# Optimization experiments

Measured on AMD Instinct MI355X. Metric: run time of the kernel, lower is better.

Reference implementation:

```python
import jax, jax.numpy as jnp
import numpy as np

B, S, D = 2, 2048, 1024
H = 16
HD = D // H
MLP = 4096
EPS_LN = 1e-6
EPS_NORM = 1e-12
LOG_MAX = float(np.log(1.0 / 0.01))  # clamp cap for logit_scale


def setup_inputs() -> dict:
    key = jax.random.key(0)
    ks = jax.random.split(key, 12)
    sd = 0.02
    return {
        "x": jax.random.normal(ks[0], (B, S, D), jnp.float32),
        "wq": jax.random.normal(ks[1], (D, D), jnp.float32) * sd,
        "bq": jnp.zeros((D,), jnp.float32),
        "wk": jax.random.normal(ks[2], (D, D), jnp.float32) * sd,
        "bk": jnp.zeros((D,), jnp.float32),
        "wv": jax.random.normal(ks[3], (D, D), jnp.float32) * sd,
        "bv": jnp.zeros((D,), jnp.float32),
        "wo": jax.random.normal(ks[4], (D, D), jnp.float32) * sd,
        "bo": jnp.zeros((D,), jnp.float32),
        "w1": jax.random.normal(ks[5], (D, MLP), jnp.float32) * sd,
        "b1": jax.random.normal(ks[6], (MLP,), jnp.float32) * 1e-6,
        "w2": jax.random.normal(ks[7], (MLP, D), jnp.float32) * sd,
        "b2": jax.random.normal(ks[8], (D,), jnp.float32) * 1e-6,
        "ln1_g": jnp.ones((D,), jnp.float32),
        "ln1_b": jnp.zeros((D,), jnp.float32),
        "ln2_g": jnp.ones((D,), jnp.float32),
        "ln2_b": jnp.zeros((D,), jnp.float32),
        "logit_scale": jnp.log(10.0 * jnp.ones((H, 1, 1), jnp.float32)),
    }


def _layernorm(x, g, b):
    mu = jnp.mean(x, axis=-1, keepdims=True)
    var = jnp.var(x, axis=-1, keepdims=True)
    return (x - mu) * jax.lax.rsqrt(var + EPS_LN) * g + b


def _l2norm(x):
    n = jnp.linalg.norm(x, axis=-1, keepdims=True)
    return x / jnp.maximum(n, EPS_NORM)


def _split_heads(t):  # [B,S,D] -> [B,H,S,HD]
    return t.reshape(B, S, H, HD).transpose(0, 2, 1, 3)


def reference(x, wq, bq, wk, bk, wv, bv, wo, bo, w1, b1, w2, b2,
              ln1_g, ln1_b, ln2_g, ln2_b, logit_scale):
    h = x
    xn = _layernorm(x, ln1_g, ln1_b)
    q = _split_heads(xn @ wq + bq)
    k = _split_heads(xn @ wk + bk)
    v = _split_heads(xn @ wv + bv)
    # cosine attention: L2-normalize q,k, scale by clamped learnable exp temp
    scores = jnp.einsum("bhqd,bhkd->bhqk", _l2norm(q), _l2norm(k))
    scale = jnp.exp(jnp.minimum(logit_scale, LOG_MAX))  # [H,1,1]
    scores = scores * scale
    probs = jax.nn.softmax(scores, axis=-1)
    ctx = jnp.einsum("bhqk,bhkd->bhqd", probs, v)
    ctx = ctx.transpose(0, 2, 1, 3).reshape(B, S, D)
    x = ctx @ wo + bo + h
    h = x
    xn = _layernorm(x, ln2_g, ln2_b)
    y = jax.nn.gelu(xn @ w1 + b1, approximate=False) @ w2 + b2
    return y + h
```

## Files before the change

### kernel.cpp

```cpp
#include <hip/hip_runtime.h>
#include <hip/hip_bf16.h>
#include <math.h>

typedef unsigned short u16;
typedef unsigned int u32;
typedef __attribute__((ext_vector_type(8))) short bf16x8;
typedef __attribute__((ext_vector_type(4))) float f32x4;

#define S_LEN 2048
#define DM 1024
#define NH 16
#define HD 64
#define MLPD 4096
#define BSZ 2
#define NROWS (BSZ * S_LEN)
#define LOGMAX 4.60517018598809f

__device__ __forceinline__ u16 f2bf(float f) {
  u32 u = __float_as_uint(f);
  u32 r = (u + 0x7fffu + ((u >> 16) & 1u)) >> 16;
  return (u16)r;
}
__device__ __forceinline__ float bf2f(u16 h) { return __uint_as_float(((u32)h) << 16); }
__device__ __forceinline__ u32 pk2(float a, float b) {
  return (u32)f2bf(a) | ((u32)f2bf(b) << 16);
}
__device__ __forceinline__ void gld16(const void* g, void* l) {
  __builtin_amdgcn_global_load_lds(
      (const __attribute__((address_space(1))) void*)g,
      (__attribute__((address_space(3))) void*)l, 16, 0, 0);
}

__global__ __launch_bounds__(256) void ln_bf16(const float* __restrict__ x,
                                               const float* __restrict__ g,
                                               const float* __restrict__ b,
                                               u16* __restrict__ out) {
  const int row = blockIdx.x;
  const int t = threadIdx.x;
  const float* xr = x + (size_t)row * DM;
  float4 v = *reinterpret_cast<const float4*>(xr + t * 4);
  float s = v.x + v.y + v.z + v.w;
  float s2 = v.x * v.x + v.y * v.y + v.z * v.z + v.w * v.w;
#pragma unroll
  for (int off = 32; off > 0; off >>= 1) {
    s += __shfl_down(s, off);
    s2 += __shfl_down(s2, off);
  }
  __shared__ float red[8];
  __shared__ float mv[2];
  const int wid = t >> 6, lane = t & 63;
  if (lane == 0) { red[wid] = s; red[wid + 4] = s2; }
  __syncthreads();
  if (t == 0) {
    float ts = red[0] + red[1] + red[2] + red[3];
    float ts2 = red[4] + red[5] + red[6] + red[7];
    float mu = ts * (1.0f / DM);
    float var = ts2 * (1.0f / DM) - mu * mu;
    mv[0] = mu;
    mv[1] = rsqrtf(var + 1e-6f);
  }
  __syncthreads();
  const float mu = mv[0], rs = mv[1];
  float4 gv = *reinterpret_cast<const float4*>(g + t * 4);
  float4 bv = *reinterpret_cast<const float4*>(b + t * 4);
  float o0 = (v.x - mu) * rs * gv.x + bv.x;
  float o1 = (v.y - mu) * rs * gv.y + bv.y;
  float o2 = (v.z - mu) * rs * gv.z + bv.z;
  float o3 = (v.w - mu) * rs * gv.w + bv.w;
  uint2 o;
  o.x = pk2(o0, o1);
  o.y = pk2(o2, o3);
  *reinterpret_cast<uint2*>(out + (size_t)row * DM + t * 4) = o;
}

__global__ __launch_bounds__(256) void prep_weights(
    const float* __restrict__ wq, const float* __restrict__ wk, const float* __restrict__ wv,
    const float* __restrict__ wo, const float* __restrict__ w1, const float* __restrict__ w2,
    const float* __restrict__ bq, const float* __restrict__ bk, const float* __restrict__ bv,
    u16* __restrict__ wqkv_t, u16* __restrict__ wo_t, u16* __restrict__ w1_t,
    u16* __restrict__ w2_t, float* __restrict__ bqkv) {
  const int tid = threadIdx.x;
  int bid = blockIdx.x;
  if (bid < 12) {
    int i = bid * 256 + tid;
    bqkv[i] = i < 1024 ? bq[i] : (i < 2048 ? bk[i - 1024] : bv[i - 2048]);
  }
  const float* src;
  u16* dst;
  int K, N;
  if (bid < 768) {
    int m = bid >> 8;
    src = (m == 0) ? wq : (m == 1 ? wk : wv);
    dst = wqkv_t + (size_t)m * 1024 * 1024;
    K = 1024; N = 1024;
    bid &= 255;
  } else if (bid < 1024) {
    src = wo; dst = wo_t; K = 1024; N = 1024; bid -= 768;
  } else if (bid < 2048) {
    src = w1; dst = w1_t; K = 1024; N = 4096; bid -= 1024;
  } else {
    src = w2; dst = w2_t; K = 4096; N = 1024; bid -= 2048;
  }
  const int ktiles = K >> 6;
  const int k0 = (bid % ktiles) << 6, n0 = (bid / ktiles) << 6;
  __shared__ float tile[64][65];
#pragma unroll
  for (int p = 0; p < 4; ++p) {
    int r = p * 16 + (tid >> 4), c = (tid & 15) * 4;
    *reinterpret_cast<float4*>(&tile[r][c]) =
        *reinterpret_cast<const float4*>(&src[(size_t)(k0 + r) * N + n0 + c]);
  }
  __syncthreads();
#pragma unroll
  for (int p = 0; p < 4; ++p) {
    int n = p * 16 + (tid >> 4), k = (tid & 15) * 4;
    uint2 o;
    o.x = pk2(tile[k][n], tile[k + 1][n]);
    o.y = pk2(tile[k + 2][n], tile[k + 3][n]);
    *reinterpret_cast<uint2*>(&dst[(size_t)(n0 + n) * K + k0 + k]) = o;
  }
}

#define EPI_BIAS 0
#define EPI_GELU 1
#define EPI_RES 2
#define EPI_QKV 3

template <int EPI, int OUTBF>
__global__ __launch_bounds__(256) void gemm_bf16(
    const u16* __restrict__ A, const u16* __restrict__ Bt,
    const float* __restrict__ bias, const float* __restrict__ res,
    void* __restrict__ Cout, u16* __restrict__ qkx, u16* __restrict__ vtx,
    int M, int N, int K) {
  __shared__ u16 As[128 * 32];
  __shared__ u16 Bs[128 * 32];
  const int tid = threadIdx.x;
  const int wid = tid >> 6, lane = tid & 63;
  const int n0 = blockIdx.x * 128, m0 = blockIdx.y * 128;
  const int wr = wid >> 1, wc = wid & 1;

  f32x4 acc[4][4];
#pragma unroll
  for (int mi = 0; mi < 4; ++mi)
#pragma unroll
    for (int ni = 0; ni < 4; ++ni)
#pragma unroll
      for (int r = 0; r < 4; ++r) acc[mi][ni][r] = 0.0f;

  const int srow = lane >> 2;
  const int skc = (lane & 3) * 8;

  for (int k0 = 0; k0 < K; k0 += 32) {
#pragma unroll
    for (int i = 0; i < 2; ++i) {
      int c = wid * 2 + i;
      gld16(&A[(size_t)(m0 + c * 16 + srow) * K + k0 + skc], &As[c * 512]);
      gld16(&Bt[(size_t)(n0 + c * 16 + srow) * K + k0 + skc], &Bs[c * 512]);
    }
    __syncthreads();
    const int fr = lane & 15, fg = (lane >> 4) * 8;
    bf16x8 af[4], bfr[4];
#pragma unroll
    for (int mi = 0; mi < 4; ++mi)
      af[mi] = *reinterpret_cast<const bf16x8*>(&As[(wr * 64 + mi * 16 + fr) * 32 + fg]);
#pragma unroll
    for (int ni = 0; ni < 4; ++ni)
      bfr[ni] = *reinterpret_cast<const bf16x8*>(&Bs[(wc * 64 + ni * 16 + fr) * 32 + fg]);
#pragma unroll
    for (int mi = 0; mi < 4; ++mi)
#pragma unroll
      for (int ni = 0; ni < 4; ++ni)
        acc[mi][ni] =
            __builtin_amdgcn_mfma_f32_16x16x32_bf16(af[mi], bfr[ni], acc[mi][ni], 0, 0, 0);
    __syncthreads();
  }

  const int col0 = n0 + wc * 64 + (lane & 15);
  const int r4 = (lane >> 4) * 4;

  if constexpr (EPI == EPI_QKV) {
    float bias4[4];
#pragma unroll
    for (int ni = 0; ni < 4; ++ni) bias4[ni] = bias[col0 + ni * 16];
    const bool isV = (n0 + wc * 64) >= 2048;
#pragma unroll
    for (int mi = 0; mi < 4; ++mi) {
#pragma unroll
      for (int r = 0; r < 4; ++r) {
        const int row = m0 + wr * 64 + mi * 16 + r4 + r;
        float v[4];
#pragma unroll
        for (int ni = 0; ni < 4; ++ni) v[ni] = acc[mi][ni][r] + bias4[ni];
        if (!isV) {
          float ss = v[0] * v[0] + v[1] * v[1] + v[2] * v[2] + v[3] * v[3];
          ss += __shfl_xor(ss, 1);
          ss += __shfl_xor(ss, 2);
          ss += __shfl_xor(ss, 4);
          ss += __shfl_xor(ss, 8);
          float inv = 1.0f / fmaxf(sqrtf(ss), 1e-12f);
#pragma unroll
          for (int ni = 0; ni < 4; ++ni)
            qkx[(size_t)row * 2048 + col0 + ni * 16] = f2bf(v[ni] * inv);
        } else {
          const int b = row >> 11, sl = row & 2047;
#pragma unroll
          for (int ni = 0; ni < 4; ++ni) {
            const int col = col0 + ni * 16;
            const int h = (col - 2048) >> 6, d = col & 63;
            vtx[((size_t)(b * NH + h) * HD + d) * S_LEN + sl] = f2bf(v[ni]);
          }
        }
      }
    }
    return;
  }

  float bias8[4];
#pragma unroll
  for (int ni = 0; ni < 4; ++ni) bias8[ni] = bias[col0 + ni * 16];
#pragma unroll
  for (int ni = 0; ni < 4; ++ni) {
    const int col = col0 + ni * 16;
    const float bb = bias8[ni];
#pragma unroll
    for (int mi = 0; mi < 4; ++mi) {
      const int row = m0 + wr * 64 + mi * 16 + r4;
#pragma unroll
      for (int r = 0; r < 4; ++r) {
        float v = acc[mi][ni][r] + bb;
        if (EPI == EPI_GELU) v = 0.5f * v * (1.0f + erff(v * 0.70710678118654752f));
        if (EPI == EPI_RES) v += res[(size_t)(row + r) * N + col];
        if (OUTBF)
          ((u16*)Cout)[(size_t)(row + r) * N + col] = f2bf(v);
        else
          ((float*)Cout)[(size_t)(row + r) * N + col] = v;
      }
    }
  }
}

__global__ __launch_bounds__(256) void flash_mfma(const u16* __restrict__ qk,
                                                  const u16* __restrict__ vt,
                                                  const float* __restrict__ lsc,
                                                  u16* __restrict__ ctx) {
  __shared__ u16 Ks[64 * 72];
  __shared__ u16 Vt[64 * 72];
  __shared__ u16 Ps[128 * 72];
  const int tid = threadIdx.x;
  const int wq = tid >> 6, lane = tid & 63;
  const int q0 = blockIdx.x * 128;
  const int bh = blockIdx.y, b = bh >> 4, h = bh & 15;
  const float scale = __expf(fminf(lsc[h], LOGMAX));
  const int fr = lane & 15, fgq = lane >> 4;

  bf16x8 qf[2][2];
#pragma unroll
  for (int qs = 0; qs < 2; ++qs)
#pragma unroll
    for (int ds = 0; ds < 2; ++ds)
      qf[qs][ds] = *reinterpret_cast<const bf16x8*>(
          &qk[(size_t)(b * S_LEN + q0 + wq * 32 + qs * 16 + fr) * 2048 + h * HD + ds * 32 +
              fgq * 8]);

  float den[2][4];
  f32x4 octx[2][4];
#pragma unroll
  for (int qs = 0; qs < 2; ++qs)
#pragma unroll
    for (int r = 0; r < 4; ++r) {
      den[qs][r] = 0.0f;
      octx[qs][r][0] = octx[qs][r][1] = octx[qs][r][2] = octx[qs][r][3] = 0.0f;
    }

  const int sr = tid >> 2, sseg = tid & 3;

  for (int kt = 0; kt < S_LEN / 64; ++kt) {
    {
      const u16* gkp = qk + (size_t)(b * S_LEN + kt * 64 + sr) * 2048 + 1024 + h * HD + sseg * 8;
      *reinterpret_cast<uint4*>(&Ks[sr * 72 + sseg * 8]) =
          *reinterpret_cast<const uint4*>(gkp);
      *reinterpret_cast<uint4*>(&Ks[sr * 72 + 32 + sseg * 8]) =
          *reinterpret_cast<const uint4*>(gkp + 32);
      const u16* gvp = vt + (size_t)(bh * HD + sr) * S_LEN + kt * 64 + sseg * 8;
      *reinterpret_cast<uint4*>(&Vt[sr * 72 + sseg * 8]) =
          *reinterpret_cast<const uint4*>(gvp);
      *reinterpret_cast<uint4*>(&Vt[sr * 72 + 32 + sseg * 8]) =
          *reinterpret_cast<const uint4*>(gvp + 32);
    }
    __syncthreads();

    f32x4 sc[2][4];
#pragma unroll
    for (int qs = 0; qs < 2; ++qs)
#pragma unroll
      for (int ks = 0; ks < 4; ++ks)
        sc[qs][ks][0] = sc[qs][ks][1] = sc[qs][ks][2] = sc[qs][ks][3] = 0.0f;
#pragma unroll
    for (int ks = 0; ks < 4; ++ks)
#pragma unroll
      for (int ds = 0; ds < 2; ++ds) {
        bf16x8 kf = *reinterpret_cast<const bf16x8*>(&Ks[(ks * 16 + fr) * 72 + ds * 32 + fgq * 8]);
#pragma unroll
        for (int qs = 0; qs < 2; ++qs)
          sc[qs][ks] = __builtin_amdgcn_mfma_f32_16x16x32_bf16(qf[qs][ds], kf, sc[qs][ks], 0, 0, 0);
      }

#pragma unroll
    for (int qs = 0; qs < 2; ++qs)
#pragma unroll
      for (int r = 0; r < 4; ++r) {
        const int prow = wq * 32 + qs * 16 + fgq * 4 + r;
        float ps = 0.0f;
#pragma unroll
        for (int ks = 0; ks < 4; ++ks) {
          float p = __expf(scale * (sc[qs][ks][r] - 1.0f));
          Ps[prow * 72 + ks * 16 + fr] = f2bf(p);
          ps += p;
        }
        ps += __shfl_xor(ps, 1);
        ps += __shfl_xor(ps, 2);
        ps += __shfl_xor(ps, 4);
        ps += __shfl_xor(ps, 8);
        den[qs][r] += ps;
      }

#pragma unroll
    for (int kvs = 0; kvs < 2; ++kvs) {
      bf16x8 pf0 = *reinterpret_cast<const bf16x8*>(&Ps[(wq * 32 + fr) * 72 + kvs * 32 + fgq * 8]);
      bf16x8 pf1 =
          *reinterpret_cast<const bf16x8*>(&Ps[(wq * 32 + 16 + fr) * 72 + kvs * 32 + fgq * 8]);
#pragma unroll
      for (int dsb = 0; dsb < 4; ++dsb) {
        bf16x8 vf = *reinterpret_cast<const bf16x8*>(&Vt[(dsb * 16 + fr) * 72 + kvs * 32 + fgq * 8]);
        octx[0][dsb] = __builtin_amdgcn_mfma_f32_16x16x32_bf16(pf0, vf, octx[0][dsb], 0, 0, 0);
        octx[1][dsb] = __builtin_amdgcn_mfma_f32_16x16x32_bf16(pf1, vf, octx[1][dsb], 0, 0, 0);
      }
    }
    __syncthreads();
  }

#pragma unroll
  for (int qs = 0; qs < 2; ++qs)
#pragma unroll
    for (int r = 0; r < 4; ++r) {
      float inv = 1.0f / den[qs][r];
      const int row = q0 + wq * 32 + qs * 16 + fgq * 4 + r;
#pragma unroll
      for (int dsb = 0; dsb < 4; ++dsb)
        ctx[(size_t)(b * S_LEN + row) * DM + h * HD + dsb * 16 + fr] =
            f2bf(octx[qs][dsb][r] * inv);
    }
}

extern "C" void kernel_launch(void* const* d_in, const int* in_sizes, int n_in,
                              void* d_out, int out_size, void* d_ws, size_t ws_size,
                              hipStream_t stream) {
  const float* x    = (const float*)d_in[0];
  const float* wq   = (const float*)d_in[1];
  const float* bq   = (const float*)d_in[2];
  const float* wk   = (const float*)d_in[3];
  const float* bk   = (const float*)d_in[4];
  const float* wv   = (const float*)d_in[5];
  const float* bv   = (const float*)d_in[6];
  const float* wo   = (const float*)d_in[7];
  const float* bo   = (const float*)d_in[8];
  const float* w1   = (const float*)d_in[9];
  const float* b1   = (const float*)d_in[10];
  const float* w2   = (const float*)d_in[11];
  const float* b2   = (const float*)d_in[12];
  const float* ln1g = (const float*)d_in[13];
  const float* ln1b = (const float*)d_in[14];
  const float* ln2g = (const float*)d_in[15];
  const float* ln2b = (const float*)d_in[16];
  const float* lsc  = (const float*)d_in[17];

  char* ws = (char*)d_ws;
  u16* wqkv_t = (u16*)(ws + 0);
  u16* wo_t   = (u16*)(ws + 6291456);
  u16* w1_t   = (u16*)(ws + 8388608);
  u16* w2_t   = (u16*)(ws + 16777216);
  float* bqkv = (float*)(ws + 25165824);
  u16* xn     = (u16*)(ws + 25178112);
  float* x2   = (float*)(ws + 33566720);
  u16* qkbuf  = (u16*)(ws + 50343936);
  u16* vtbuf  = (u16*)(ws + 67121152);
  u16* ctx    = (u16*)(ws + 75509760);
  u16* h1     = qkbuf;

  prep_weights<<<dim3(3072), dim3(256), 0, stream>>>(wq, wk, wv, wo, w1, w2, bq, bk, bv,
                                                     wqkv_t, wo_t, w1_t, w2_t, bqkv);
  ln_bf16<<<dim3(NROWS), dim3(256), 0, stream>>>(x, ln1g, ln1b, xn);
  gemm_bf16<EPI_QKV, 1><<<dim3(3072 / 128, NROWS / 128), dim3(256), 0, stream>>>(
      xn, wqkv_t, bqkv, nullptr, nullptr, qkbuf, vtbuf, NROWS, 3072, 1024);
  flash_mfma<<<dim3(S_LEN / 128, BSZ * NH), dim3(256), 0, stream>>>(qkbuf, vtbuf, lsc, ctx);
  gemm_bf16<EPI_RES, 0><<<dim3(1024 / 128, NROWS / 128), dim3(256), 0, stream>>>(
      ctx, wo_t, bo, x, x2, nullptr, nullptr, NROWS, 1024, 1024);
  ln_bf16<<<dim3(NROWS), dim3(256), 0, stream>>>(x2, ln2g, ln2b, xn);
  gemm_bf16<EPI_GELU, 1><<<dim3(4096 / 128, NROWS / 128), dim3(256), 0, stream>>>(
      xn, w1_t, b1, nullptr, h1, nullptr, nullptr, NROWS, 4096, 1024);
  gemm_bf16<EPI_RES, 0><<<dim3(1024 / 128, NROWS / 128), dim3(256), 0, stream>>>(
      h1, w2_t, b2, x2, (float*)d_out, nullptr, nullptr, NROWS, 1024, 4096);
}
```

Before: 481.3 us.

## Rework flash attention with 32x32 MFMA, register P, and double-buffered K/V

```diff
diff --git a/kernel.cpp b/kernel.cpp
--- a/kernel.cpp
+++ b/kernel.cpp
@@ -6,6 +6,7 @@
 typedef unsigned int u32;
 typedef __attribute__((ext_vector_type(8))) short bf16x8;
 typedef __attribute__((ext_vector_type(4))) float f32x4;
+typedef __attribute__((ext_vector_type(16))) float f32x16;
 
 #define S_LEN 2048
 #define DM 1024
@@ -24,6 +25,11 @@
 __device__ __forceinline__ float bf2f(u16 h) { return __uint_as_float(((u32)h) << 16); }
 __device__ __forceinline__ u32 pk2(float a, float b) {
   return (u32)f2bf(a) | ((u32)f2bf(b) << 16);
+}
+__device__ __forceinline__ u32 cvtpk(float a, float b) {
+  u32 r;
+  asm("v_cvt_pk_bf16_f32 %0, %1, %2" : "=v"(r) : "v"(a), "v"(b));
+  return r;
 }
 __device__ __forceinline__ void gld16(const void* g, void* l) {
   __builtin_amdgcn_global_load_lds(
@@ -243,113 +249,131 @@
                                                   const u16* __restrict__ vt,
                                                   const float* __restrict__ lsc,
                                                   u16* __restrict__ ctx) {
-  __shared__ u16 Ks[64 * 72];
-  __shared__ u16 Vt[64 * 72];
-  __shared__ u16 Ps[128 * 72];
+  __shared__ u16 Ks[2][64 * 72];
+  __shared__ u16 Vt[2][64 * 72];
+  __shared__ float den_s[128];
   const int tid = threadIdx.x;
   const int wq = tid >> 6, lane = tid & 63;
+  const int lo5 = lane & 31, hi = lane >> 5;
   const int q0 = blockIdx.x * 128;
   const int bh = blockIdx.y, b = bh >> 4, h = bh & 15;
   const float scale = __expf(fminf(lsc[h], LOGMAX));
-  const int fr = lane & 15, fgq = lane >> 4;
-
-  bf16x8 qf[2][2];
-#pragma unroll
-  for (int qs = 0; qs < 2; ++qs)
-#pragma unroll
-    for (int ds = 0; ds < 2; ++ds)
-      qf[qs][ds] = *reinterpret_cast<const bf16x8*>(
-          &qk[(size_t)(b * S_LEN + q0 + wq * 32 + qs * 16 + fr) * 2048 + h * HD + ds * 32 +
-              fgq * 8]);
-
-  float den[2][4];
-  f32x4 octx[2][4];
-#pragma unroll
-  for (int qs = 0; qs < 2; ++qs)
-#pragma unroll
-    for (int r = 0; r < 4; ++r) {
-      den[qs][r] = 0.0f;
-      octx[qs][r][0] = octx[qs][r][1] = octx[qs][r][2] = octx[qs][r][3] = 0.0f;
+
+  bf16x8 qf[4];
+#pragma unroll
+  for (int dch = 0; dch < 4; ++dch)
+    qf[dch] = *reinterpret_cast<const bf16x8*>(
+        &qk[(size_t)(b * S_LEN + q0 + wq * 32 + lo5) * 2048 + h * HD + dch * 16 + hi * 8]);
+
+  f32x16 octx[2];
+#pragma unroll
+  for (int dt = 0; dt < 2; ++dt)
+#pragma unroll
+    for (int e = 0; e < 16; ++e) octx[dt][e] = 0.0f;
+  float den = 0.0f;
+
+  const int sr = tid >> 2, sseg = tid & 3;
+  const u16* kbase = qk + (size_t)(b * S_LEN + sr) * 2048 + 1024 + h * HD + sseg * 8;
+  const u16* vbase = vt + (size_t)(bh * HD + sr) * S_LEN + sseg * 8;
+
+  {
+    uint4 k0 = *reinterpret_cast<const uint4*>(kbase);
+    uint4 k1 = *reinterpret_cast<const uint4*>(kbase + 32);
+    uint4 v0 = *reinterpret_cast<const uint4*>(vbase);
+    uint4 v1 = *reinterpret_cast<const uint4*>(vbase + 32);
+    *reinterpret_cast<uint4*>(&Ks[0][sr * 72 + sseg * 8]) = k0;
+    *reinterpret_cast<uint4*>(&Ks[0][sr * 72 + 32 + sseg * 8]) = k1;
+    *reinterpret_cast<uint4*>(&Vt[0][sr * 72 + sseg * 8]) = v0;
+    *reinterpret_cast<uint4*>(&Vt[0][sr * 72 + 32 + sseg * 8]) = v1;
+  }
+  __syncthreads();
+
+  int buf = 0;
+  for (int kt = 0; kt < S_LEN / 64; ++kt) {
+    const int nx = (kt + 1) & (S_LEN / 64 - 1);
+    uint4 k0 = *reinterpret_cast<const uint4*>(kbase + (size_t)nx * 64 * 2048);
+    uint4 k1 = *reinterpret_cast<const uint4*>(kbase + (size_t)nx * 64 * 2048 + 32);
+    uint4 v0 = *reinterpret_cast<const uint4*>(vbase + nx * 64);
+    uint4 v1 = *reinterpret_cast<const uint4*>(vbase + nx * 64 + 32);
+
+    const u16* Kc = &Ks[buf][0];
+    const u16* Vc = &Vt[buf][0];
+
+    f32x16 sc[2];
+#pragma unroll
+    for (int ktile = 0; ktile < 2; ++ktile)
+#pragma unroll
+      for (int e = 0; e < 16; ++e) sc[ktile][e] = 0.0f;
+#pragma unroll
+    for (int ktile = 0; ktile < 2; ++ktile)
+#pragma unroll
+      for (int dch = 0; dch < 4; ++dch) {
+        bf16x8 kf = *reinterpret_cast<const bf16x8*>(
+            &Kc[(ktile * 32 + lo5) * 72 + dch * 16 + hi * 8]);
+        sc[ktile] = __builtin_amdgcn_mfma_f32_32x32x16_bf16(kf, qf[dch], sc[ktile], 0, 0, 0);
+      }
+
+    u32 pk[2][8];
+    float ps = 0.0f;
+#pragma unroll
+    for (int ktile = 0; ktile < 2; ++ktile) {
+      float p[16];
+#pragma unroll
+      for (int r = 0; r < 16; ++r) {
+        p[r] = __expf(fmaf(scale, sc[ktile][r], -scale));
+        ps += p[r];
+      }
+#pragma unroll
+      for (int n = 0; n < 4; ++n) {
+        pk[ktile][n * 2] = cvtpk(p[n * 4], p[n * 4 + 1]);
+        pk[ktile][n * 2 + 1] = cvtpk(p[n * 4 + 2], p[n * 4 + 3]);
+      }
     }
-
-  const int sr = tid >> 2, sseg = tid & 3;
-
-  for (int kt = 0; kt < S_LEN / 64; ++kt) {
-    {
-      const u16* gkp = qk + (size_t)(b * S_LEN + kt * 64 + sr) * 2048 + 1024 + h * HD + sseg * 8;
-      *reinterpret_cast<uint4*>(&Ks[sr * 72 + sseg * 8]) =
-          *reinterpret_cast<const uint4*>(gkp);
-      *reinterpret_cast<uint4*>(&Ks[sr * 72 + 32 + sseg * 8]) =
-          *reinterpret_cast<const uint4*>(gkp + 32);
-      const u16* gvp = vt + (size_t)(bh * HD + sr) * S_LEN + kt * 64 + sseg * 8;
-      *reinterpret_cast<uint4*>(&Vt[sr * 72 + sseg * 8]) =
-          *reinterpret_cast<const uint4*>(gvp);
-      *reinterpret_cast<uint4*>(&Vt[sr * 72 + 32 + sseg * 8]) =
-          *reinterpret_cast<const uint4*>(gvp + 32);
-    }
+    ps += __shfl_xor(ps, 32);
+    den += ps;
+
+#pragma unroll
+    for (int ktile = 0; ktile < 2; ++ktile)
+#pragma unroll
+      for (int cc = 0; cc < 2; ++cc) {
+        u32 o0 = pk[ktile][(2 * cc) * 2], o1 = pk[ktile][(2 * cc) * 2 + 1];
+        u32 e0 = pk[ktile][(2 * cc + 1) * 2], e1 = pk[ktile][(2 * cc + 1) * 2 + 1];
+        u32 s0 = (u32)__shfl_xor((int)o0, 32);
+        u32 s1 = (u32)__shfl_xor((int)o1, 32);
+        u32 t0 = (u32)__shfl_xor((int)e0, 32);
+        u32 t1 = (u32)__shfl_xor((int)e1, 32);
+        union { u32 u[4]; bf16x8 v; } pf;
+        pf.u[0] = hi ? t0 : o0;
+        pf.u[1] = hi ? t1 : o1;
+        pf.u[2] = hi ? e0 : s0;
+        pf.u[3] = hi ? e1 : s1;
+        const int kvo = (ktile * 2 + cc) * 16 + hi * 8;
+#pragma unroll
+        for (int dt = 0; dt < 2; ++dt) {
+          bf16x8 vf = *reinterpret_cast<const bf16x8*>(&Vc[(dt * 32 + lo5) * 72 + kvo]);
+          octx[dt] = __builtin_amdgcn_mfma_f32_32x32x16_bf16(pf.v, vf, octx[dt], 0, 0, 0);
+        }
+      }
+
+    *reinterpret_cast<uint4*>(&Ks[buf ^ 1][sr * 72 + sseg * 8]) = k0;
+    *reinterpret_cast<uint4*>(&Ks[buf ^ 1][sr * 72 + 32 + sseg * 8]) = k1;
+    *reinterpret_cast<uint4*>(&Vt[buf ^ 1][sr * 72 + sseg * 8]) = v0;
+    *reinterpret_cast<uint4*>(&Vt[buf ^ 1][sr * 72 + 32 + sseg * 8]) = v1;
     __syncthreads();
-
-    f32x4 sc[2][4];
-#pragma unroll
-    for (int qs = 0; qs < 2; ++qs)
-#pragma unroll
-      for (int ks = 0; ks < 4; ++ks)
-        sc[qs][ks][0] = sc[qs][ks][1] = sc[qs][ks][2] = sc[qs][ks][3] = 0.0f;
-#pragma unroll
-    for (int ks = 0; ks < 4; ++ks)
-#pragma unroll
-      for (int ds = 0; ds < 2; ++ds) {
-        bf16x8 kf = *reinterpret_cast<const bf16x8*>(&Ks[(ks * 16 + fr) * 72 + ds * 32 + fgq * 8]);
-#pragma unroll
-        for (int qs = 0; qs < 2; ++qs)
-          sc[qs][ks] = __builtin_amdgcn_mfma_f32_16x16x32_bf16(qf[qs][ds], kf, sc[qs][ks], 0, 0, 0);
-      }
-
-#pragma unroll
-    for (int qs = 0; qs < 2; ++qs)
-#pragma unroll
-      for (int r = 0; r < 4; ++r) {
-        const int prow = wq * 32 + qs * 16 + fgq * 4 + r;
-        float ps = 0.0f;
-#pragma unroll
-        for (int ks = 0; ks < 4; ++ks) {
-          float p = __expf(scale * (sc[qs][ks][r] - 1.0f));
-          Ps[prow * 72 + ks * 16 + fr] = f2bf(p);
-          ps += p;
-        }
-        ps += __shfl_xor(ps, 1);
-        ps += __shfl_xor(ps, 2);
-        ps += __shfl_xor(ps, 4);
-        ps += __shfl_xor(ps, 8);
-        den[qs][r] += ps;
-      }
-
-#pragma unroll
-    for (int kvs = 0; kvs < 2; ++kvs) {
-      bf16x8 pf0 = *reinterpret_cast<const bf16x8*>(&Ps[(wq * 32 + fr) * 72 + kvs * 32 + fgq * 8]);
-      bf16x8 pf1 =
-          *reinterpret_cast<const bf16x8*>(&Ps[(wq * 32 + 16 + fr) * 72 + kvs * 32 + fgq * 8]);
-#pragma unroll
-      for (int dsb = 0; dsb < 4; ++dsb) {
-        bf16x8 vf = *reinterpret_cast<const bf16x8*>(&Vt[(dsb * 16 + fr) * 72 + kvs * 32 + fgq * 8]);
-        octx[0][dsb] = __builtin_amdgcn_mfma_f32_16x16x32_bf16(pf0, vf, octx[0][dsb], 0, 0, 0);
-        octx[1][dsb] = __builtin_amdgcn_mfma_f32_16x16x32_bf16(pf1, vf, octx[1][dsb], 0, 0, 0);
-      }
-    }
-    __syncthreads();
-  }
-
-#pragma unroll
-  for (int qs = 0; qs < 2; ++qs)
-#pragma unroll
-    for (int r = 0; r < 4; ++r) {
-      float inv = 1.0f / den[qs][r];
-      const int row = q0 + wq * 32 + qs * 16 + fgq * 4 + r;
-#pragma unroll
-      for (int dsb = 0; dsb < 4; ++dsb)
-        ctx[(size_t)(b * S_LEN + row) * DM + h * HD + dsb * 16 + fr] =
-            f2bf(octx[qs][dsb][r] * inv);
-    }
+    buf ^= 1;
+  }
+
+  if (hi == 0) den_s[wq * 32 + lo5] = den;
+  __syncthreads();
+#pragma unroll
+  for (int r = 0; r < 16; ++r) {
+    const int ql = (r & 3) + 8 * (r >> 2) + 4 * hi;
+    const float inv = 1.0f / den_s[wq * 32 + ql];
+    const size_t row = (size_t)(b * S_LEN + q0 + wq * 32 + ql);
+#pragma unroll
+    for (int dt = 0; dt < 2; ++dt)
+      ctx[row * DM + h * HD + dt * 32 + lo5] = f2bf(octx[dt][r] * inv);
+  }
 }
 
 extern "C" void kernel_launch(void* const* d_in, const int* in_sizes, int n_in,
```

Result: faster. 441.9 us (-8.2%).
